# Optimization experiments

Measured on AMD Instinct MI355X. Metric: run time of the kernel, lower is better.

Reference implementation:

```python
import jax, jax.numpy as jnp
from jax import lax
import numpy as np

WS = 8        # window size
SHIFT = 4     # shift size
HEADS = 4
EPS = 1e-5


def _rel_pos_index(ws):
    coords = np.stack(np.meshgrid(np.arange(ws), np.arange(ws), indexing='ij'))  # (2,ws,ws)
    cf = coords.reshape(2, -1)
    rel = cf[:, :, None] - cf[:, None, :]           # (2,n,n)
    rel = rel.transpose(1, 2, 0).astype(np.int64)   # (n,n,2)
    rel[:, :, 0] += ws - 1
    rel[:, :, 1] += ws - 1
    rel[:, :, 0] *= 2 * ws - 1
    return rel.sum(-1)                              # (n,n)


def _attn_mask(h, w, ws, ss):
    img = np.zeros((h, w), dtype=np.float32)
    cnt = 0
    for hs in (slice(0, -ws), slice(-ws, -ss), slice(-ss, None)):
        for wsl in (slice(0, -ws), slice(-ws, -ss), slice(-ss, None)):
            img[hs, wsl] = cnt
            cnt += 1
    mw = img.reshape(h // ws, ws, w // ws, ws).transpose(0, 2, 1, 3).reshape(-1, ws * ws)
    am = mw[:, None, :] - mw[:, :, None]            # (nW,n,n)
    return np.where(am != 0, -100.0, 0.0).astype(np.float32)


def _ln(x, w, b):
    mu = x.mean(-1, keepdims=True)
    var = jnp.var(x, axis=-1, keepdims=True)
    return (x - mu) * lax.rsqrt(var + EPS) * w + b


def setup_inputs() -> dict:
    key = jax.random.key(0)
    ks = jax.random.split(key, 16)
    b, c, h, w = 4, 64, 256, 256
    hidden = 4 * c
    n_bias = (2 * WS - 1) * (2 * WS - 1)
    s = 0.02
    return {
        'x': jax.random.normal(ks[0], (b, c, h, w), jnp.float32),
        'norm1_w': jnp.ones((c,), jnp.float32),
        'norm1_b': jnp.zeros((c,), jnp.float32),
        'qkv_w': jax.random.normal(ks[1], (3 * c, c), jnp.float32) * s,
        'qkv_b': jnp.zeros((3 * c,), jnp.float32),
        'rpb': jax.random.normal(ks[2], (n_bias, HEADS), jnp.float32) * s,
        'proj_w': jax.random.normal(ks[3], (c, c), jnp.float32) * s,
        'proj_b': jnp.zeros((c,), jnp.float32),
        'norm2_w': jnp.ones((c,), jnp.float32),
        'norm2_b': jnp.zeros((c,), jnp.float32),
        'fc1_w': jax.random.normal(ks[4], (hidden, c), jnp.float32) * s,
        'fc1_b': jnp.zeros((hidden,), jnp.float32),
        'dw_w': jax.random.normal(ks[5], (hidden, 1, 5, 5), jnp.float32) * s,
        'dw_b': jnp.zeros((hidden,), jnp.float32),
        'fc2_w': jax.random.normal(ks[6], (c, hidden), jnp.float32) * s,
        'fc2_b': jnp.zeros((c,), jnp.float32),
    }


def reference(x, norm1_w, norm1_b, qkv_w, qkv_b, rpb, proj_w, proj_b,
              norm2_w, norm2_b, fc1_w, fc1_b, dw_w, dw_b, fc2_w, fc2_b):
    b, c, h, w = x.shape
    d = c // HEADS
    scale = d ** (-0.5)
    n = WS * WS

    x3 = jnp.transpose(x.reshape(b, c, h * w), (0, 2, 1))  # (b, hw, c)
    shortcut = x3
    xn = _ln(x3, norm1_w, norm1_b).reshape(b, h, w, c)

    # cyclic shift + window partition
    sx = jnp.roll(xn, (-SHIFT, -SHIFT), axis=(1, 2))
    win = sx.reshape(b, h // WS, WS, w // WS, WS, c).transpose(0, 1, 3, 2, 4, 5).reshape(-1, n, c)
    B_ = win.shape[0]

    qkv = (win @ qkv_w.T + qkv_b).reshape(B_, n, 3, HEADS, d).transpose(2, 0, 3, 1, 4)
    q, k, v = qkv[0] * scale, qkv[1], qkv[2]   # (B_, H, n, d)
    attn = jnp.einsum('bhnd,bhmd->bhnm', q, k)  # (B_, H, n, n)

    bias = rpb[jnp.asarray(_rel_pos_index(WS)).reshape(-1)].reshape(n, n, HEADS).transpose(2, 0, 1)
    attn = attn + bias[None]

    mask = jnp.asarray(_attn_mask(h, w, WS, SHIFT))  # (nW, n, n)
    nW = mask.shape[0]
    attn = attn.reshape(B_ // nW, nW, HEADS, n, n) + mask[None, :, None]
    attn = jax.nn.softmax(attn.reshape(B_, HEADS, n, n), axis=-1)

    out = jnp.einsum('bhnm,bhmd->bhnd', attn, v).transpose(0, 2, 1, 3).reshape(B_, n, c)
    out = out @ proj_w.T + proj_b

    # window reverse + un-shift
    sx = out.reshape(b, h // WS, w // WS, WS, WS, c).transpose(0, 1, 3, 2, 4, 5).reshape(b, h, w, c)
    xr = jnp.roll(sx, (SHIFT, SHIFT), axis=(1, 2)).reshape(b, h * w, c)
    x3 = shortcut + xr

    # ConvFFN
    xn = _ln(x3, norm2_w, norm2_b)
    hid = jax.nn.gelu(xn @ fc1_w.T + fc1_b, approximate=False)  # (b, hw, hidden)
    hidden = hid.shape[-1]
    himg = hid.transpose(0, 2, 1).reshape(b, hidden, h, w)
    dc = lax.conv_general_dilated(himg, dw_w, (1, 1), [(2, 2), (2, 2)],
                                  dimension_numbers=('NCHW', 'OIHW', 'NCHW'),
                                  feature_group_count=hidden)
    dc = jax.nn.gelu(dc + dw_b[None, :, None, None], approximate=False)
    hid = hid + dc.reshape(b, hidden, h * w).transpose(0, 2, 1)
    x3 = x3 + (hid @ fc2_w.T + fc2_b)

    return jnp.transpose(x3, (0, 2, 1)).reshape(b, c, h, w)
```

## Files before the change

### kernel.cpp

```cpp
#include <hip/hip_runtime.h>
#include <hip/hip_bf16.h>
#include <hip/hip_fp8.h>
#include <math.h>


typedef __bf16  bf16x8  __attribute__((ext_vector_type(8)));
typedef float   f32x4   __attribute__((ext_vector_type(4)));
typedef float   f32x2   __attribute__((ext_vector_type(2)));
typedef unsigned short ushortx8 __attribute__((ext_vector_type(8)));

__device__ __forceinline__ float gelu_f(float v) {
    float u = v * fmaf(0.0713548354f, v * v, 1.5957691216f);
    float t = __expf(u);
    float r = __builtin_amdgcn_rcpf(t + 1.0f);
    return v - v * r;
}
__device__ __forceinline__ unsigned char f32_to_fp8(float v) {
    __hip_fp8_e4m3 t(v);
    return (unsigned char)t.__x;
}
__device__ __forceinline__ float fp8_to_f32(unsigned char u) {
    __hip_fp8_e4m3 t;
    t.__x = (__hip_fp8_storage_t)u;
    return (float)t;
}

#if __has_builtin(__builtin_amdgcn_cvt_pk_f32_fp8) && __has_builtin(__builtin_amdgcn_cvt_pk_fp8_f32)
#define HW_FP8 1
#endif
template<bool HI>
__device__ __forceinline__ f32x2 fp8x2_f32(unsigned int u) {
#ifdef HW_FP8
    return __builtin_amdgcn_cvt_pk_f32_fp8((int)u, HI);
#else
    f32x2 r;
    const int s = HI ? 16 : 0;
    r.x = fp8_to_f32((unsigned char)(u >> s));
    r.y = fp8_to_f32((unsigned char)(u >> (s + 8)));
    return r;
#endif
}
template<bool HI>
__device__ __forceinline__ unsigned int f32x2_fp8(float a, float b, unsigned int old) {
#ifdef HW_FP8
    return (unsigned int)__builtin_amdgcn_cvt_pk_fp8_f32(a, b, (int)old, HI);
#else
    unsigned int v = (unsigned int)f32_to_fp8(a) | ((unsigned int)f32_to_fp8(b) << 8);
    return HI ? ((old & 0x0000ffffu) | (v << 16)) : ((old & 0xffff0000u) | v);
#endif
}

__device__ __forceinline__ unsigned short f2bf(float f) {
    unsigned int u = __builtin_bit_cast(unsigned int, f);
    u += 0x7fffu + ((u >> 16) & 1u);
    return (unsigned short)(u >> 16);
}
__device__ __forceinline__ float bf2f(unsigned short u) {
    return __builtin_bit_cast(float, ((unsigned int)u) << 16);
}
__device__ __forceinline__ unsigned int cvt_pk_bf16(float a, float b) {
#if defined(__gfx950__)
    unsigned int r;
    asm("v_cvt_pk_bf16_f32 %0, %1, %2" : "=v"(r) : "v"(a), "v"(b));
    return r;
#else
    return (unsigned int)f2bf(a) | ((unsigned int)f2bf(b) << 16);
#endif
}

__global__ __launch_bounds__(256) void k_prep(
        const float* __restrict__ qkvw, const float* __restrict__ projw,
        const float* __restrict__ rpb,  const float* __restrict__ fc1w,
        unsigned short* __restrict__ qkvw_bf, unsigned short* __restrict__ projw_bf,
        unsigned short* __restrict__ rpb_bf,  unsigned short* __restrict__ fc1w_bf) {
    const int i = blockIdx.x * 256 + threadIdx.x;
    if (i < 12288) qkvw_bf[i] = f2bf(qkvw[i]);
    if (i < 4096)  projw_bf[i] = f2bf(projw[i]);
    if (i < 900)   rpb_bf[i]   = f2bf(rpb[i]);
    if (i < 16384) fc1w_bf[i]  = f2bf(fc1w[i]);
}

__global__ __launch_bounds__(256) void k_cvt(const float* __restrict__ src,
        unsigned short* __restrict__ dst, int n) {
    const int i = blockIdx.x * 256 + threadIdx.x;
    if (i < n) dst[i] = f2bf(src[i]);
}

__global__ __launch_bounds__(256) void k_ln1(const float* __restrict__ x,
        const float* __restrict__ w1, const float* __restrict__ b1,
        unsigned short* __restrict__ A, unsigned short* __restrict__ Bw) {
    __shared__ float tile[64 * 65];
    __shared__ float red0[256], red1[256];
    __shared__ float muv[64], rsv[64], lw[64], lb[64];
    const int tid = threadIdx.x;
    const int gid = blockIdx.x;
    const int xc = gid & 3, y = (gid >> 2) & 255, b = gid >> 10;
    const int x0 = xc * 64;
    if (tid < 64) { lw[tid] = w1[tid]; lb[tid] = b1[tid]; }

    const float* xb = x + ((size_t)b * 64) * 65536 + y * 256 + x0;
    {
        const int tk = tid & 63, cl = tid >> 6;
        for (int it = 0; it < 16; ++it) {
            int cc = cl + 4 * it;
            tile[cc * 65 + tk] = xb[(size_t)cc * 65536 + tk];
        }
    }
    __syncthreads();
    {
        const int tk = tid & 63, cl = tid >> 6;
        float s = 0.f, s2 = 0.f;
        #pragma unroll
        for (int k = 0; k < 16; ++k) {
            float v = tile[(cl * 16 + k) * 65 + tk];
            s += v; s2 += v * v;
        }
        red0[cl * 64 + tk] = s; red1[cl * 64 + tk] = s2;
    }
    __syncthreads();
    if (tid < 64) {
        float s  = red0[tid] + red0[64 + tid] + red0[128 + tid] + red0[192 + tid];
        float s2 = red1[tid] + red1[64 + tid] + red1[128 + tid] + red1[192 + tid];
        float mu = s * (1.f / 64.f);
        float var = s2 * (1.f / 64.f) - mu * mu;
        muv[tid] = mu; rsv[tid] = rsqrtf(var + 1e-5f);
    }
    __syncthreads();
    const int cp = tid & 31, ch0 = cp * 2;
    const int tl = tid >> 5;
    const float2 lwp = *(const float2*)&lw[ch0];
    const float2 lbp = *(const float2*)&lb[ch0];
    const int ys = (y + 252) & 255;
    const int wy = ys >> 3, py = ys & 7;
    #pragma unroll
    for (int it = 0; it < 8; ++it) {
        const int t = tl + 8 * it;
        const float v0 = tile[ch0 * 65 + t];
        const float v1 = tile[(ch0 + 1) * 65 + t];
        const int tok = (b << 16) + y * 256 + x0 + t;
        *(unsigned int*)&A[(size_t)tok * 64 + ch0] = cvt_pk_bf16(v0, v1);
        const float mu = muv[t], rs = rsv[t];
        const float vn0 = (v0 - mu) * rs * lwp.x + lbp.x;
        const float vn1 = (v1 - mu) * rs * lwp.y + lbp.y;
        const int xs = (x0 + t + 252) & 255;
        const int wx = xs >> 3, px = xs & 7;
        const int widx = (b << 10) + (wy << 5) + wx;
        const int pos = (py << 3) + px;
        *(unsigned int*)&Bw[((size_t)widx * 64 + pos) * 64 + ch0] = cvt_pk_bf16(vn0, vn1);
    }
}

__global__ __launch_bounds__(256) void k_attn(
        const unsigned short* __restrict__ Bw,
        const unsigned short* __restrict__ qkvw_bf,
        const unsigned short* __restrict__ projw_bf,
        const unsigned short* __restrict__ rpb_bf,
        const float* __restrict__ qkvb,
        const float* __restrict__ projb,
        const unsigned short* __restrict__ A, unsigned short* __restrict__ Cb) {
    __shared__ __align__(16) unsigned short Xs[4608];
    __shared__ __align__(16) unsigned short Ws[13824];
    __shared__ __align__(8)  unsigned short rpbl[900];
    __shared__ float qkvbl[192];
    __shared__ float projbl[64];

    const int tid = threadIdx.x;
    const int lane = tid & 63, wv = tid >> 6;
    const int l15 = lane & 15, quad = lane >> 4;
    const int widx = blockIdx.x;
    const int wib = widx & 1023;
    const int wy = wib >> 5, wx = wib & 31, bimg = widx >> 10;
    const bool edge = (wy == 31) | (wx == 31);

    const f32x4 zz = {0.f, 0.f, 0.f, 0.f};
    const ushortx8 zu = {0, 0, 0, 0, 0, 0, 0, 0};
    const bf16x8 z8 = __builtin_bit_cast(bf16x8, zu);
    const ushortx8 ou = {0x3F80, 0x3F80, 0x3F80, 0x3F80, 0x3F80, 0x3F80, 0x3F80, 0x3F80};
    const bf16x8 ones8 = __builtin_bit_cast(bf16x8, ou);

    const ushortx8 pw0 = *(const ushortx8*)(projw_bf + tid * 8);
    const ushortx8 pw1 = *(const ushortx8*)(projw_bf + (256 + tid) * 8);

    {
        const unsigned short* Xg = Bw + (size_t)widx * 4096 + wv * 1024;
        #pragma unroll
        for (int it = 0; it < 2; ++it) {
            int g = it * 64 + lane;
            int row = g >> 3, c8 = g & 7;
            *(ushortx8*)&Xs[(wv * 16 + row) * 72 + c8 * 8] =
                *(const ushortx8*)(Xg + g * 8);
        }
    }
    #pragma unroll
    for (int it = 0; it < 6; ++it) {
        int g = it * 256 + tid;
        int row = g >> 3, c8 = g & 7;
        *(ushortx8*)&Ws[row * 72 + c8 * 8] = *(const ushortx8*)(qkvw_bf + g * 8);
    }
    if (tid < 225) *(uint2*)&rpbl[tid * 4] = *(const uint2*)(rpb_bf + tid * 4);
    if (tid < 192) qkvbl[tid] = qkvb[tid];
    if (tid < 64)  projbl[tid] = projb[tid];
    __syncthreads();

    f32x4 qacc[12];
    #pragma unroll
    for (int i = 0; i < 12; ++i) qacc[i] = zz;
    {
        const bf16x8 av0 = *(const bf16x8*)&Xs[(16 * wv + l15) * 72 + quad * 8];
        const bf16x8 av1 = *(const bf16x8*)&Xs[(16 * wv + l15) * 72 + 32 + quad * 8];
        #pragma unroll
        for (int gl = 0; gl < 12; ++gl) {
            bf16x8 bv0 = *(const bf16x8*)&Ws[(gl * 16 + l15) * 72 + quad * 8];
            qacc[gl] = __builtin_amdgcn_mfma_f32_16x16x32_bf16(av0, bv0, qacc[gl], 0, 0, 0);
            bf16x8 bv1 = *(const bf16x8*)&Ws[(gl * 16 + l15) * 72 + 32 + quad * 8];
            qacc[gl] = __builtin_amdgcn_mfma_f32_16x16x32_bf16(av1, bv1, qacc[gl], 0, 0, 0);
        }
    }
    __syncthreads();

    #pragma unroll
    for (int g = 0; g < 12; ++g) {
        #pragma unroll
        for (int r = 0; r < 4; ++r) {
            int tok = 16 * wv + quad * 4 + r;
            int oc  = g * 16 + l15;
            float v = qacc[g][r] + qkvbl[oc];
            if (g < 4)       Ws[g * 1024 + tok * 16 + l15] = f2bf(v * 0.25f);
            else if (g < 8)  Ws[4096 + (g - 4) * 1024 + tok * 16 + l15] = f2bf(v);
            else             Ws[8192 + ((g - 8) * 16 + l15) * 72 + tok] = f2bf(v);
        }
    }
    __syncthreads();

    f32x4 sacc[4][4];
    #pragma unroll
    for (int h = 0; h < 4; ++h) {
        bf16x8 qa = z8;
        if (quad < 2) qa = *(const bf16x8*)&Ws[h * 1024 + (16 * wv + l15) * 16 + quad * 8];
        #pragma unroll
        for (int nt = 0; nt < 4; ++nt) {
            bf16x8 kf = z8;
            if (quad < 2) kf = *(const bf16x8*)&Ws[4096 + h * 1024 + (nt * 16 + l15) * 16 + quad * 8];
            sacc[h][nt] = __builtin_amdgcn_mfma_f32_16x16x32_bf16(qa, kf, zz, 0, 0, 0);
        }
    }
    __syncthreads();

    {
        const int r0 = tid >> 3;
        *(ushortx8*)&Ws[4096 + r0 * 64 + (((tid & 7) ^ (r0 & 7)) << 3)] = pw0;
        const int g1 = 256 + tid, r1 = g1 >> 3;
        *(ushortx8*)&Ws[4096 + r1 * 64 + (((g1 & 7) ^ (r1 & 7)) << 3)] = pw1;
    }

    const int jhi = l15 >> 3, jlo = l15 & 7;
    int offj4[4], regj[4];
    #pragma unroll
    for (int nt = 0; nt < 4; ++nt) {
        int j = nt * 16 + l15;
        int jy = j >> 3, jx = j & 7;
        offj4[nt] = (jy * 15 + jx) * 4;
        regj[nt] = 0;
        if (edge) {
            int ysj = wy * 8 + jy, xsj = wx * 8 + jx;
            regj[nt] = (ysj >= 252 ? 2 : (ysj >= 248 ? 1 : 0)) * 3
                     + (xsj >= 252 ? 2 : (xsj >= 248 ? 1 : 0));
        }
    }
    int rbA[4], regiA[4], pbaseA[4], i7A[4];
    #pragma unroll
    for (int r = 0; r < 4; ++r) {
        const int i = 16 * wv + quad * 4 + r;
        const int iy = i >> 3, ix = i & 7;
        rbA[r] = ((iy + 7) * 15 + (ix + 7)) * 4;
        i7A[r] = i & 7;
        pbaseA[r] = i * 64 + jlo;
        regiA[r] = 0;
        if (edge) {
            const int ysi = wy * 8 + iy, xsi = wx * 8 + ix;
            regiA[r] = (ysi >= 252 ? 2 : (ysi >= 248 ? 1 : 0)) * 3
                     + (xsi >= 252 ? 2 : (xsi >= 248 ? 1 : 0));
        }
    }

    #pragma unroll
    for (int r = 0; r < 4; ++r) {
        #pragma unroll
        for (int nt = 0; nt < 4; ++nt) {
            const uint2 bw = *(const uint2*)&rpbl[rbA[r] - offj4[nt]];
            float mk = 0.f;
            if (edge) mk = (regj[nt] == regiA[r]) ? 0.f : -100.f;
            sacc[0][nt][r] += __builtin_bit_cast(float, bw.x << 16) + mk;
            sacc[1][nt][r] += __builtin_bit_cast(float, bw.x & 0xffff0000u) + mk;
            sacc[2][nt][r] += __builtin_bit_cast(float, bw.y << 16) + mk;
            sacc[3][nt][r] += __builtin_bit_cast(float, bw.y & 0xffff0000u) + mk;
        }
    }
    int pA_[4][4];
    #pragma unroll
    for (int r = 0; r < 4; ++r)
        #pragma unroll
        for (int nt = 0; nt < 4; ++nt)
            pA_[r][nt] = pbaseA[r] + ((((nt << 1) | jhi) ^ i7A[r]) << 3);

    f32x4 o[4];
    #pragma unroll
    for (int h = 0; h < 4; ++h) {
        #pragma unroll
        for (int r = 0; r < 4; ++r) {
            const unsigned int pk01 = cvt_pk_bf16(__expf(sacc[h][0][r]),
                                                  __expf(sacc[h][1][r]));
            const unsigned int pk23 = cvt_pk_bf16(__expf(sacc[h][2][r]),
                                                  __expf(sacc[h][3][r]));
            Ws[pA_[r][0]] = (unsigned short)pk01;
            Ws[pA_[r][1]] = (unsigned short)(pk01 >> 16);
            Ws[pA_[r][2]] = (unsigned short)pk23;
            Ws[pA_[r][3]] = (unsigned short)(pk23 >> 16);
        }
        o[h] = zz;
        f32x4 os = zz;
        #pragma unroll
        for (int s = 0; s < 2; ++s) {
            bf16x8 pa = *(const bf16x8*)&Ws[(16 * wv + l15) * 64
                                            + (((s * 4 + quad) ^ (l15 & 7)) << 3)];
            bf16x8 vb = *(const bf16x8*)&Ws[8192 + (h * 16 + l15) * 72 + s * 32 + quad * 8];
            o[h] = __builtin_amdgcn_mfma_f32_16x16x32_bf16(pa, vb, o[h], 0, 0, 0);
            os   = __builtin_amdgcn_mfma_f32_16x16x32_bf16(pa, ones8, os, 0, 0, 0);
        }
        #pragma unroll
        for (int r = 0; r < 4; ++r) o[h][r] *= __builtin_amdgcn_rcpf(os[r]);
    }

    unsigned short resid[16];
    #pragma unroll
    for (int r = 0; r < 4; ++r) {
        int tok = 16 * wv + quad * 4 + r;
        int py = tok >> 3, px = tok & 7;
        int yo = (wy * 8 + py + 4) & 255, xo = (wx * 8 + px + 4) & 255;
        size_t gt = ((size_t)bimg << 16) + yo * 256 + xo;
        #pragma unroll
        for (int nt = 0; nt < 4; ++nt)
            resid[r * 4 + nt] = A[gt * 64 + nt * 16 + l15];
    }

    #pragma unroll
    for (int h = 0; h < 4; ++h)
        #pragma unroll
        for (int r = 0; r < 4; ++r)
            Xs[(16 * wv + quad * 4 + r) * 72 + h * 16 + l15] = f2bf(o[h][r]);
    __syncthreads();

    f32x4 pacc[4];
    #pragma unroll
    for (int nt = 0; nt < 4; ++nt) {
        pacc[nt] = zz;
        #pragma unroll
        for (int s = 0; s < 2; ++s) {
            bf16x8 oa = *(const bf16x8*)&Xs[(16 * wv + l15) * 72 + s * 32 + quad * 8];
            bf16x8 wb = *(const bf16x8*)&Ws[4096 + (nt * 16 + l15) * 64
                                            + (((s * 4 + quad) ^ (l15 & 7)) << 3)];
            pacc[nt] = __builtin_amdgcn_mfma_f32_16x16x32_bf16(oa, wb, pacc[nt], 0, 0, 0);
        }
    }

    #pragma unroll
    for (int r = 0; r < 4; ++r) {
        int tok = 16 * wv + quad * 4 + r;
        int py = tok >> 3, px = tok & 7;
        int yo = (wy * 8 + py + 4) & 255, xo = (wx * 8 + px + 4) & 255;
        size_t gt = ((size_t)bimg << 16) + yo * 256 + xo;
        #pragma unroll
        for (int nt = 0; nt < 4; ++nt) {
            int oc = nt * 16 + l15;
            float v = pacc[nt][r] + projbl[oc] + bf2f(resid[r * 4 + nt]);
            Cb[gt * 64 + oc] = f2bf(v);
        }
    }
}

__global__ __launch_bounds__(256) void k_ln2fc1(const unsigned short* __restrict__ Cb,
        const float* __restrict__ w2, const float* __restrict__ b2,
        const unsigned short* __restrict__ fc1w_bf, const float* __restrict__ fc1b,
        unsigned char* __restrict__ D) {
    __shared__ __align__(16) unsigned short Xb[64 * 72];
    __shared__ __align__(16) unsigned short Wb[256 * 72];
    __shared__ float red0[256], red1[256];
    __shared__ float muv[64], rsv[64], lwv[64], lbv[64], fb[256];
    const int tid = threadIdx.x, gid = blockIdx.x;
    const int xc = gid & 3, y = (gid >> 2) & 255, b = gid >> 10;
    const int x0 = xc * 64;
    const int lane = tid & 63, wv = tid >> 6;
    const int l15 = lane & 15, quad = lane >> 4;
    const f32x4 zz = {0.f, 0.f, 0.f, 0.f};

    if (tid < 64) { lwv[tid] = w2[tid]; lbv[tid] = b2[tid]; }
    fb[tid] = fc1b[tid];

    const unsigned short* Cp = Cb + ((size_t)(b << 16) + y * 256 + x0) * 64;
    #pragma unroll
    for (int it = 0; it < 2; ++it) {
        const int g = it * 256 + tid;
        const int row = g >> 3, c8 = g & 7;
        *(ushortx8*)&Xb[row * 72 + c8 * 8] = *(const ushortx8*)(Cp + g * 8);
    }
    {
        const ushortx8* w8 = (const ushortx8*)fc1w_bf;
        #pragma unroll
        for (int it = 0; it < 8; ++it) {
            int idx = it * 256 + tid;
            int row = idx >> 3, c8 = idx & 7;
            *(ushortx8*)&Wb[row * 72 + c8 * 8] = w8[idx];
        }
    }
    __syncthreads();
    {
        const int tok = tid & 63, cl = tid >> 6;
        float s = 0.f, s2 = 0.f;
        #pragma unroll
        for (int g = 0; g < 2; ++g) {
            const ushortx8 u = *(const ushortx8*)&Xb[tok * 72 + cl * 16 + g * 8];
            #pragma unroll
            for (int k = 0; k < 8; ++k) { float v = bf2f(u[k]); s += v; s2 += v * v; }
        }
        red0[cl * 64 + tok] = s; red1[cl * 64 + tok] = s2;
    }
    __syncthreads();
    if (tid < 64) {
        float s  = red0[tid] + red0[64 + tid] + red0[128 + tid] + red0[192 + tid];
        float s2 = red1[tid] + red1[64 + tid] + red1[128 + tid] + red1[192 + tid];
        float mu = s * (1.f / 64.f);
        float var = s2 * (1.f / 64.f) - mu * mu;
        muv[tid] = mu; rsv[tid] = rsqrtf(var + 1e-5f);
    }
    __syncthreads();
    {
        const int c8n = tid & 7;
        const float4 lwa = *(const float4*)&lwv[c8n * 8];
        const float4 lwb2 = *(const float4*)&lwv[c8n * 8 + 4];
        const float4 lba = *(const float4*)&lbv[c8n * 8];
        const float4 lbb2 = *(const float4*)&lbv[c8n * 8 + 4];
        const float lw8[8] = {lwa.x, lwa.y, lwa.z, lwa.w, lwb2.x, lwb2.y, lwb2.z, lwb2.w};
        const float lb8[8] = {lba.x, lba.y, lba.z, lba.w, lbb2.x, lbb2.y, lbb2.z, lbb2.w};
        #pragma unroll
        for (int it = 0; it < 2; ++it) {
            const int row = it * 32 + (tid >> 3);
            const ushortx8 u = *(const ushortx8*)&Xb[row * 72 + c8n * 8];
            const float mu = muv[row], rs = rsv[row];
            float v[8];
            #pragma unroll
            for (int k = 0; k < 8; ++k) v[k] = (bf2f(u[k]) - mu) * rs * lw8[k] + lb8[k];
            uint4 pk;
            pk.x = cvt_pk_bf16(v[0], v[1]); pk.y = cvt_pk_bf16(v[2], v[3]);
            pk.z = cvt_pk_bf16(v[4], v[5]); pk.w = cvt_pk_bf16(v[6], v[7]);
            *(uint4*)&Xb[row * 72 + c8n * 8] = pk;
        }
    }
    __syncthreads();

    f32x4 acc[4][4];
    #pragma unroll
    for (int mt = 0; mt < 4; ++mt)
        #pragma unroll
        for (int nt = 0; nt < 4; ++nt) acc[mt][nt] = zz;
    #pragma unroll
    for (int s = 0; s < 2; ++s) {
        bf16x8 Bf[4];
        #pragma unroll
        for (int nt = 0; nt < 4; ++nt)
            Bf[nt] = *(const bf16x8*)&Xb[(nt * 16 + l15) * 72 + s * 32 + quad * 8];
        #pragma unroll
        for (int mt = 0; mt < 4; ++mt) {
            bf16x8 Af = *(const bf16x8*)&Wb[(64 * wv + 16 * mt + l15) * 72 + s * 32 + quad * 8];
            #pragma unroll
            for (int nt = 0; nt < 4; ++nt)
                acc[mt][nt] = __builtin_amdgcn_mfma_f32_16x16x32_bf16(Af, Bf[nt], acc[mt][nt], 0, 0, 0);
        }
    }

    unsigned int* stT = (unsigned int*)&Wb[(size_t)(64 * wv) * 72];
    const int s4 = lane >> 4;
    #pragma unroll
    for (int mt = 0; mt < 4; ++mt) {
        #pragma unroll
        for (int r = 0; r < 4; ++r) {
            const int mch = 64 * wv + 16 * mt + quad * 4 + r;
            const float bias = fb[mch];
            float g0 = gelu_f(acc[mt][0][r] + bias);
            float g1 = gelu_f(acc[mt][1][r] + bias);
            float g2 = gelu_f(acc[mt][2][r] + bias);
            float g3 = gelu_f(acc[mt][3][r] + bias);
            unsigned int pk = f32x2_fp8<false>(g0, g1, 0u);
            pk = f32x2_fp8<true>(g2, g3, pk);
            stT[(quad * 4 + r) * 20 + l15] = pk;
        }
        const int orow = l15;
        const uint4 w = *(const uint4*)&stT[orow * 20 + 4 * s4];
        const int mch2 = 64 * wv + 16 * mt + orow;
        unsigned char* Dp2 = D + (((size_t)(b * 256 + mch2)) << 16) + y * 256 + x0;
        #pragma unroll
        for (int p = 0; p < 4; ++p) {
            unsigned int o = ((w.x >> (8 * p)) & 0xffu)
                           | (((w.y >> (8 * p)) & 0xffu) << 8)
                           | (((w.z >> (8 * p)) & 0xffu) << 16)
                           | (((w.w >> (8 * p)) & 0xffu) << 24);
            *(unsigned int*)&Dp2[16 * p + 4 * s4] = o;
        }
    }
}

__global__ __launch_bounds__(256) void k_dwconv(const unsigned char* __restrict__ D,
        const float* __restrict__ dww, const float* __restrict__ dwb,
        unsigned char* __restrict__ E) {
    __shared__ __align__(16) unsigned short inT[36 * 280 + 16];
    __shared__ __align__(16) unsigned short Atab[5 * 64 * 8];
    __shared__ __align__(16) unsigned char outT[4][16 * 144];
    const int tid = threadIdx.x, gid = blockIdx.x;
    const int yt = gid & 7, pc = gid >> 3;
    const int ch = pc & 255;
    const int y0 = yt * 32;
    const unsigned char* Dp = D + ((size_t)pc << 16);
    const f32x4 zz = {0.f, 0.f, 0.f, 0.f};

    for (int idx = tid; idx < 432; idx += 256) {
        const int r = idx / 12, c = idx - r * 12;
        const int dw = (c == 0) ? 0 : (128 + c);
        ((unsigned int*)&inT[r * 280])[dw] = 0u;
    }
    #pragma unroll
    for (int it = 0; it < 9; ++it) {
        const int u = it * 256 + tid;
        const int t = u >> 6, c = u & 63;
        const int gy = y0 - 2 + t;
        unsigned int v = 0u;
        if ((unsigned)gy < 256u) v = *(const unsigned int*)(Dp + gy * 256 + 4 * c);
        const f32x2 lo = fp8x2_f32<false>(v);
        const f32x2 hi = fp8x2_f32<true>(v);
        unsigned int* base = (unsigned int*)&inT[t * 280 + 2 + 4 * c];
        base[0] = cvt_pk_bf16(lo.x, lo.y);
        base[1] = cvt_pk_bf16(hi.x, hi.y);
    }
    #pragma unroll
    for (int q = 0; q < 10; ++q) {
        const int e = tid * 10 + q;
        const int ky = e >> 9, r = e & 511;
        const int l = r >> 3, j = r & 7;
        const int m = l & 15, k = ((l >> 4) << 3) + j;
        const int d = k - m;
        float wv = 0.f;
        if (d >= 0 && d < 5) wv = dww[ch * 25 + ky * 5 + d];
        Atab[e] = f2bf(wv);
    }
    const float bb = dwb[ch];
    __syncthreads();

    const int wv_ = tid >> 6, lane = tid & 63;
    const int l15 = lane & 15, quad = lane >> 4;
    const int g = wv_ >> 1, xh = wv_ & 1;
    bf16x8 Af[5];
    #pragma unroll
    for (int ky = 0; ky < 5; ++ky)
        Af[ky] = *(const bf16x8*)&Atab[(ky * 64 + lane) * 8];
    const int tbase = g * 16 + l15;

    #pragma unroll
    for (int xp = 0; xp < 8; ++xp) {
        const int xs = xh * 128 + xp * 16;
        f32x4 acc = zz;
        #pragma unroll
        for (int ky = 0; ky < 5; ++ky) {
            bf16x8 Bf = *(const bf16x8*)&inT[(tbase + ky) * 280 + xs + quad * 8];
            acc = __builtin_amdgcn_mfma_f32_16x16x32_bf16(Af[ky], Bf, acc, 0, 0, 0);
        }
        const unsigned int* cp32 = (const unsigned int*)&inT[(tbase + 2) * 280 + 2 + xs + quad * 4];
        const unsigned int c01 = cp32[0], c23 = cp32[1];
        const float c0 = bf2f((unsigned short)c01), c1 = bf2f((unsigned short)(c01 >> 16));
        const float c2 = bf2f((unsigned short)c23), c3 = bf2f((unsigned short)(c23 >> 16));
        unsigned int pk = f32x2_fp8<false>(c0 + gelu_f(acc[0] + bb), c1 + gelu_f(acc[1] + bb), 0u);
        pk = f32x2_fp8<true>(c2 + gelu_f(acc[2] + bb), c3 + gelu_f(acc[3] + bb), pk);
        *(unsigned int*)&outT[wv_][l15 * 144 + xp * 16 + quad * 4] = pk;
    }

    {
        const int row = lane >> 2, sg = lane & 3;
        unsigned char* Ep = E + ((size_t)pc << 16) + (y0 + g * 16 + row) * 256 + xh * 128 + sg * 32;
        *(uint4*)Ep        = *(const uint4*)&outT[wv_][row * 144 + sg * 32];
        *(uint4*)(Ep + 16) = *(const uint4*)&outT[wv_][row * 144 + sg * 32 + 16];
    }
}

__global__ __launch_bounds__(256) void k_fc2(const unsigned char* __restrict__ E,
        const unsigned short* __restrict__ Cb, const unsigned short* __restrict__ fc2w_bf,
        const float* __restrict__ fc2b, float* __restrict__ out) {
    __shared__ __align__(16) unsigned short Hb[64 * 136];
    __shared__ __align__(16) unsigned short Wb2[64 * 264];
    __shared__ __align__(16) unsigned short Cl[64 * 72];
    __shared__ float fbl[64];
    const int tid = threadIdx.x, gid = blockIdx.x;
    const int xc = gid & 3, y = (gid >> 2) & 255, b = gid >> 10;
    const int x0 = xc * 64;
    const int lane = tid & 63, wv = tid >> 6;
    const int l15 = lane & 15, quad = lane >> 4;
    const f32x4 zz = {0.f, 0.f, 0.f, 0.f};

    if (tid < 64) fbl[tid] = fc2b[tid];
    {
        const unsigned short* Cp = Cb + ((size_t)(b << 16) + y * 256 + x0) * 64;
        #pragma unroll
        for (int it = 0; it < 2; ++it) {
            const int g = it * 256 + tid;
            const int row = g >> 3, c8 = g & 7;
            *(ushortx8*)&Cl[row * 72 + c8 * 8] = *(const ushortx8*)(Cp + g * 8);
        }
    }
    {
        const ushortx8* w8 = (const ushortx8*)fc2w_bf;
        #pragma unroll
        for (int it = 0; it < 8; ++it) {
            int idx = it * 256 + tid;
            int row = idx >> 5, c8 = idx & 31;
            *(ushortx8*)&Wb2[row * 264 + c8 * 8] = w8[idx];
        }
    }

    f32x4 acc[4];
    #pragma unroll
    for (int nt = 0; nt < 4; ++nt) acc[nt] = zz;

    const int ldc = tid >> 4;
    const int tq  = tid & 15;
    unsigned int u0[8];
    #pragma unroll
    for (int it = 0; it < 8; ++it) {
        int chl = ldc + 16 * it;
        u0[it] = *(const unsigned int*)&E[(((size_t)(b * 256 + chl)) << 16) + y * 256 + x0 + 4 * tq];
    }
    __syncthreads();

    for (int kc = 0; kc < 2; ++kc) {
        #pragma unroll
        for (int it = 0; it < 8; ++it) {
            int chl = ldc + 16 * it;
            f32x2 lo = fp8x2_f32<false>(u0[it]);
            f32x2 hi = fp8x2_f32<true>(u0[it]);
            const unsigned int p01 = cvt_pk_bf16(lo.x, lo.y);
            const unsigned int p23 = cvt_pk_bf16(hi.x, hi.y);
            unsigned short hs[4] = {(unsigned short)p01, (unsigned short)(p01 >> 16),
                                    (unsigned short)p23, (unsigned short)(p23 >> 16)};
            #pragma unroll
            for (int j = 0; j < 4; ++j) {
                int tok = 4 * tq + j;
                int p = (((chl >> 3) ^ (tok >> 2)) << 3) + (chl & 7);
                Hb[tok * 136 + p] = hs[j];
            }
        }
        if (kc == 0) {
            #pragma unroll
            for (int it = 0; it < 8; ++it) {
                int chl = ldc + 16 * it + 128;
                u0[it] = *(const unsigned int*)&E[(((size_t)(b * 256 + chl)) << 16) + y * 256 + x0 + 4 * tq];
            }
        }
        __syncthreads();
        #pragma unroll
        for (int k32 = 0; k32 < 4; ++k32) {
            bf16x8 Af = *(const bf16x8*)&Wb2[(16 * wv + l15) * 264 + kc * 128 + k32 * 32 + quad * 8];
            const int g = k32 * 4 + quad;
            #pragma unroll
            for (int nt = 0; nt < 4; ++nt) {
                const int tok = nt * 16 + l15;
                bf16x8 Bf = *(const bf16x8*)&Hb[tok * 136 + ((g ^ (tok >> 2)) << 3)];
                acc[nt] = __builtin_amdgcn_mfma_f32_16x16x32_bf16(Af, Bf, acc[nt], 0, 0, 0);
            }
        }
        if (kc == 0) __syncthreads();
    }

    #pragma unroll
    for (int r = 0; r < 4; ++r) {
        const int oc = 16 * wv + quad * 4 + r;
        const float bias = fbl[oc];
        float* op = out + (((size_t)(b * 64 + oc)) << 16) + y * 256 + x0;
        #pragma unroll
        for (int nt = 0; nt < 4; ++nt) {
            const int tok = nt * 16 + l15;
            op[tok] = acc[nt][r] + bias + bf2f(Cl[tok * 72 + oc]);
        }
    }
}

extern "C" void kernel_launch(void* const* d_in, const int* in_sizes, int n_in,
                              void* d_out, int out_size, void* d_ws, size_t ws_size,
                              hipStream_t stream) {
    const float* x     = (const float*)d_in[0];
    const float* n1w   = (const float*)d_in[1];
    const float* n1b   = (const float*)d_in[2];
    const float* qkvw  = (const float*)d_in[3];
    const float* qkvb  = (const float*)d_in[4];
    const float* rpb   = (const float*)d_in[5];
    const float* projw = (const float*)d_in[6];
    const float* projb = (const float*)d_in[7];
    const float* n2w   = (const float*)d_in[8];
    const float* n2b   = (const float*)d_in[9];
    const float* fc1w  = (const float*)d_in[10];
    const float* fc1b  = (const float*)d_in[11];
    const float* dww   = (const float*)d_in[12];
    const float* dwb   = (const float*)d_in[13];
    const float* fc2w  = (const float*)d_in[14];
    const float* fc2b  = (const float*)d_in[15];
    float* out = (float*)d_out;

    char* ws = (char*)d_ws;
    const size_t MB = 1048576;
    unsigned short* Cbuf = (unsigned short*)ws;
    unsigned short* Ab   = (unsigned short*)(ws + 32 * MB);
    unsigned short* Bwp  = (unsigned short*)(ws + 64 * MB);
    unsigned char*  Dh   = (unsigned char*)(ws + 32 * MB);
    unsigned char*  Eh   = (unsigned char*)(ws + 96 * MB);

    unsigned short* qkvw_bf = (unsigned short*)(ws + 96 * MB);
    unsigned short* projw_bf = (unsigned short*)(ws + 96 * MB + 24576);
    unsigned short* rpb_bf   = (unsigned short*)(ws + 96 * MB + 32768);
    unsigned short* fc1w_bf  = (unsigned short*)(ws + 96 * MB + 34816);
    unsigned short* fc2w_bf  = (unsigned short*)(ws + 32 * MB);

    k_prep  <<<64,    256, 0, stream>>>(qkvw, projw, rpb, fc1w,
                                        qkvw_bf, projw_bf, rpb_bf, fc1w_bf);
    k_ln1   <<<4096,  256, 0, stream>>>(x, n1w, n1b, Ab, Bwp);
    k_attn  <<<4096,  256, 0, stream>>>(Bwp, qkvw_bf, projw_bf, rpb_bf,
                                        qkvb, projb, Ab, Cbuf);
    k_ln2fc1<<<4096,  256, 0, stream>>>(Cbuf, n2w, n2b, fc1w_bf, fc1b, Dh);
    k_dwconv<<<8192,  256, 0, stream>>>(Dh, dww, dwb, Eh);
    k_cvt   <<<64,    256, 0, stream>>>(fc2w, fc2w_bf, 16384);
    k_fc2   <<<4096,  256, 0, stream>>>(Eh, Cbuf, fc2w_bf, fc2b, out);
}
```

Measured before the change: 360.1 us.

## Fuse LayerNorm1 and shifted-window gather into the attention kernel

Removes the separate k_ln1 pass. Each attention block now reads its shifted 8x8 window directly from the fp32 NCHW input, computes LayerNorm in shared memory, and keeps the raw fp32 values in registers as the residual. This drops the bf16 A and Bw intermediate buffers and their global write and read traffic, plus one launch. In exchange the attention kernel gains an extra LN phase with more barriers, and its input reads are now strided 16-byte fp32 loads across channel planes. The residual is also kept in fp32 rather than bf16, which changes numerics slightly.

New measurement: 380.3 us. 1.06x slower.

```diff
diff --git a/kernel.cpp b/kernel.cpp
--- a/kernel.cpp
+++ b/kernel.cpp
@@ -86,78 +86,15 @@
     if (i < n) dst[i] = f2bf(src[i]);
 }
 
-__global__ __launch_bounds__(256) void k_ln1(const float* __restrict__ x,
-        const float* __restrict__ w1, const float* __restrict__ b1,
-        unsigned short* __restrict__ A, unsigned short* __restrict__ Bw) {
-    __shared__ float tile[64 * 65];
-    __shared__ float red0[256], red1[256];
-    __shared__ float muv[64], rsv[64], lw[64], lb[64];
-    const int tid = threadIdx.x;
-    const int gid = blockIdx.x;
-    const int xc = gid & 3, y = (gid >> 2) & 255, b = gid >> 10;
-    const int x0 = xc * 64;
-    if (tid < 64) { lw[tid] = w1[tid]; lb[tid] = b1[tid]; }
-
-    const float* xb = x + ((size_t)b * 64) * 65536 + y * 256 + x0;
-    {
-        const int tk = tid & 63, cl = tid >> 6;
-        for (int it = 0; it < 16; ++it) {
-            int cc = cl + 4 * it;
-            tile[cc * 65 + tk] = xb[(size_t)cc * 65536 + tk];
-        }
-    }
-    __syncthreads();
-    {
-        const int tk = tid & 63, cl = tid >> 6;
-        float s = 0.f, s2 = 0.f;
-        #pragma unroll
-        for (int k = 0; k < 16; ++k) {
-            float v = tile[(cl * 16 + k) * 65 + tk];
-            s += v; s2 += v * v;
-        }
-        red0[cl * 64 + tk] = s; red1[cl * 64 + tk] = s2;
-    }
-    __syncthreads();
-    if (tid < 64) {
-        float s  = red0[tid] + red0[64 + tid] + red0[128 + tid] + red0[192 + tid];
-        float s2 = red1[tid] + red1[64 + tid] + red1[128 + tid] + red1[192 + tid];
-        float mu = s * (1.f / 64.f);
-        float var = s2 * (1.f / 64.f) - mu * mu;
-        muv[tid] = mu; rsv[tid] = rsqrtf(var + 1e-5f);
-    }
-    __syncthreads();
-    const int cp = tid & 31, ch0 = cp * 2;
-    const int tl = tid >> 5;
-    const float2 lwp = *(const float2*)&lw[ch0];
-    const float2 lbp = *(const float2*)&lb[ch0];
-    const int ys = (y + 252) & 255;
-    const int wy = ys >> 3, py = ys & 7;
-    #pragma unroll
-    for (int it = 0; it < 8; ++it) {
-        const int t = tl + 8 * it;
-        const float v0 = tile[ch0 * 65 + t];
-        const float v1 = tile[(ch0 + 1) * 65 + t];
-        const int tok = (b << 16) + y * 256 + x0 + t;
-        *(unsigned int*)&A[(size_t)tok * 64 + ch0] = cvt_pk_bf16(v0, v1);
-        const float mu = muv[t], rs = rsv[t];
-        const float vn0 = (v0 - mu) * rs * lwp.x + lbp.x;
-        const float vn1 = (v1 - mu) * rs * lwp.y + lbp.y;
-        const int xs = (x0 + t + 252) & 255;
-        const int wx = xs >> 3, px = xs & 7;
-        const int widx = (b << 10) + (wy << 5) + wx;
-        const int pos = (py << 3) + px;
-        *(unsigned int*)&Bw[((size_t)widx * 64 + pos) * 64 + ch0] = cvt_pk_bf16(vn0, vn1);
-    }
-}
-
 __global__ __launch_bounds__(256) void k_attn(
-        const unsigned short* __restrict__ Bw,
+        const float* __restrict__ x,
+        const float* __restrict__ n1w, const float* __restrict__ n1b,
         const unsigned short* __restrict__ qkvw_bf,
         const unsigned short* __restrict__ projw_bf,
         const unsigned short* __restrict__ rpb_bf,
         const float* __restrict__ qkvb,
         const float* __restrict__ projb,
-        const unsigned short* __restrict__ A, unsigned short* __restrict__ Cb) {
+        unsigned short* __restrict__ Cb) {
     __shared__ __align__(16) unsigned short Xs[4608];
     __shared__ __align__(16) unsigned short Ws[13824];
     __shared__ __align__(8)  unsigned short rpbl[900];
@@ -178,28 +115,92 @@
     const ushortx8 ou = {0x3F80, 0x3F80, 0x3F80, 0x3F80, 0x3F80, 0x3F80, 0x3F80, 0x3F80};
     const bf16x8 ones8 = __builtin_bit_cast(bf16x8, ou);
 
+    float* rawT = (float*)Ws;
+    float* red0 = (float*)Xs;
+    float* red1 = red0 + 256;
+    float* lnw  = qkvbl;
+    float* lnb  = qkvbl + 64;
+    float* rsv  = qkvbl + 128;
+    float* muv  = projbl;
+
+    float qb = 0.f, pb = 0.f;
+    if (tid < 192) qb = qkvb[tid];
+    if (tid < 64)  pb = projb[tid];
+    if (tid < 64)  { lnw[tid] = n1w[tid]; lnb[tid] = n1b[tid]; }
+
     const ushortx8 pw0 = *(const ushortx8*)(projw_bf + tid * 8);
     const ushortx8 pw1 = *(const ushortx8*)(projw_bf + (256 + tid) * 8);
 
-    {
-        const unsigned short* Xg = Bw + (size_t)widx * 4096 + wv * 1024;
-        #pragma unroll
-        for (int it = 0; it < 2; ++it) {
-            int g = it * 64 + lane;
-            int row = g >> 3, c8 = g & 7;
-            *(ushortx8*)&Xs[(wv * 16 + row) * 72 + c8 * 8] =
-                *(const ushortx8*)(Xg + g * 8);
-        }
-    }
+    if (tid < 225) *(uint2*)&rpbl[tid * 4] = *(const uint2*)(rpb_bf + tid * 4);
+
+    {
+        const float* xb = x + (((size_t)bimg * 64) << 16);
+        #pragma unroll
+        for (int it = 0; it < 4; ++it) {
+            const int u = it * 256 + tid;
+            const int ch = u >> 4, py = (u >> 1) & 7, half = u & 1;
+            const int iy = (wy * 8 + py + 4) & 255;
+            const int col0 = (wx * 8 + 4 + half * 4) & 255;
+            const float4 v = *(const float4*)(xb + ((size_t)ch << 16) + iy * 256 + col0);
+            f32x4 w4 = {v.x, v.y, v.z, v.w};
+            *(f32x4*)&rawT[ch * 68 + py * 8 + half * 4] = w4;
+        }
+    }
+    __syncthreads();
+
+    {
+        const int tk = tid & 63, cl = tid >> 6;
+        float s = 0.f, s2 = 0.f;
+        #pragma unroll
+        for (int k = 0; k < 16; ++k) {
+            float v = rawT[(cl * 16 + k) * 68 + tk];
+            s += v; s2 += v * v;
+        }
+        red0[cl * 64 + tk] = s; red1[cl * 64 + tk] = s2;
+    }
+    __syncthreads();
+    if (tid < 64) {
+        float s  = red0[tid] + red0[64 + tid] + red0[128 + tid] + red0[192 + tid];
+        float s2 = red1[tid] + red1[64 + tid] + red1[128 + tid] + red1[192 + tid];
+        float mu = s * (1.f / 64.f);
+        float var = s2 * (1.f / 64.f) - mu * mu;
+        muv[tid] = mu; rsv[tid] = rsqrtf(var + 1e-5f);
+    }
+    __syncthreads();
+
+    {
+        const int cp = tid & 31, ch0 = cp * 2, tl = tid >> 5;
+        const float lw0 = lnw[ch0], lw1 = lnw[ch0 + 1];
+        const float lb0 = lnb[ch0], lb1 = lnb[ch0 + 1];
+        #pragma unroll
+        for (int it = 0; it < 8; ++it) {
+            const int t = tl + 8 * it;
+            const float v0 = rawT[ch0 * 68 + t];
+            const float v1 = rawT[(ch0 + 1) * 68 + t];
+            const float mu = muv[t], rs = rsv[t];
+            const float vn0 = (v0 - mu) * rs * lw0 + lb0;
+            const float vn1 = (v1 - mu) * rs * lw1 + lb1;
+            *(unsigned int*)&Xs[t * 72 + ch0] = cvt_pk_bf16(vn0, vn1);
+        }
+    }
+    float residf[16];
+    #pragma unroll
+    for (int r = 0; r < 4; ++r) {
+        const int tok = 16 * wv + quad * 4 + r;
+        #pragma unroll
+        for (int nt = 0; nt < 4; ++nt)
+            residf[r * 4 + nt] = rawT[(nt * 16 + l15) * 68 + tok];
+    }
+    __syncthreads();
+
+    if (tid < 192) qkvbl[tid] = qb;
+    if (tid < 64)  projbl[tid] = pb;
     #pragma unroll
     for (int it = 0; it < 6; ++it) {
         int g = it * 256 + tid;
         int row = g >> 3, c8 = g & 7;
         *(ushortx8*)&Ws[row * 72 + c8 * 8] = *(const ushortx8*)(qkvw_bf + g * 8);
     }
-    if (tid < 225) *(uint2*)&rpbl[tid * 4] = *(const uint2*)(rpb_bf + tid * 4);
-    if (tid < 192) qkvbl[tid] = qkvb[tid];
-    if (tid < 64)  projbl[tid] = projb[tid];
     __syncthreads();
 
     f32x4 qacc[12];
@@ -331,7 +332,26 @@
         for (int r = 0; r < 4; ++r) o[h][r] *= __builtin_amdgcn_rcpf(os[r]);
     }
 
-    unsigned short resid[16];
+    #pragma unroll
+    for (int h = 0; h < 4; ++h)
+        #pragma unroll
+        for (int r = 0; r < 4; ++r)
+            Xs[(16 * wv + quad * 4 + r) * 72 + h * 16 + l15] = f2bf(o[h][r]);
+    __syncthreads();
+
+    f32x4 pacc[4];
+    #pragma unroll
+    for (int nt = 0; nt < 4; ++nt) {
+        pacc[nt] = zz;
+        #pragma unroll
+        for (int s = 0; s < 2; ++s) {
+            bf16x8 oa = *(const bf16x8*)&Xs[(16 * wv + l15) * 72 + s * 32 + quad * 8];
+            bf16x8 wb = *(const bf16x8*)&Ws[4096 + (nt * 16 + l15) * 64
+                                            + (((s * 4 + quad) ^ (l15 & 7)) << 3)];
+            pacc[nt] = __builtin_amdgcn_mfma_f32_16x16x32_bf16(oa, wb, pacc[nt], 0, 0, 0);
+        }
+    }
+
     #pragma unroll
     for (int r = 0; r < 4; ++r) {
         int tok = 16 * wv + quad * 4 + r;
@@ -339,40 +359,9 @@
         int yo = (wy * 8 + py + 4) & 255, xo = (wx * 8 + px + 4) & 255;
         size_t gt = ((size_t)bimg << 16) + yo * 256 + xo;
         #pragma unroll
-        for (int nt = 0; nt < 4; ++nt)
-            resid[r * 4 + nt] = A[gt * 64 + nt * 16 + l15];
-    }
-
-    #pragma unroll
-    for (int h = 0; h < 4; ++h)
-        #pragma unroll
-        for (int r = 0; r < 4; ++r)
-            Xs[(16 * wv + quad * 4 + r) * 72 + h * 16 + l15] = f2bf(o[h][r]);
-    __syncthreads();
-
-    f32x4 pacc[4];
-    #pragma unroll
-    for (int nt = 0; nt < 4; ++nt) {
-        pacc[nt] = zz;
-        #pragma unroll
-        for (int s = 0; s < 2; ++s) {
-            bf16x8 oa = *(const bf16x8*)&Xs[(16 * wv + l15) * 72 + s * 32 + quad * 8];
-            bf16x8 wb = *(const bf16x8*)&Ws[4096 + (nt * 16 + l15) * 64
-                                            + (((s * 4 + quad) ^ (l15 & 7)) << 3)];
-            pacc[nt] = __builtin_amdgcn_mfma_f32_16x16x32_bf16(oa, wb, pacc[nt], 0, 0, 0);
-        }
-    }
-
-    #pragma unroll
-    for (int r = 0; r < 4; ++r) {
-        int tok = 16 * wv + quad * 4 + r;
-        int py = tok >> 3, px = tok & 7;
-        int yo = (wy * 8 + py + 4) & 255, xo = (wx * 8 + px + 4) & 255;
-        size_t gt = ((size_t)bimg << 16) + yo * 256 + xo;
-        #pragma unroll
         for (int nt = 0; nt < 4; ++nt) {
             int oc = nt * 16 + l15;
-            float v = pacc[nt][r] + projbl[oc] + bf2f(resid[r * 4 + nt]);
+            float v = pacc[nt][r] + projbl[oc] + residf[r * 4 + nt];
             Cb[gt * 64 + oc] = f2bf(v);
         }
     }
@@ -712,8 +701,6 @@
     char* ws = (char*)d_ws;
     const size_t MB = 1048576;
     unsigned short* Cbuf = (unsigned short*)ws;
-    unsigned short* Ab   = (unsigned short*)(ws + 32 * MB);
-    unsigned short* Bwp  = (unsigned short*)(ws + 64 * MB);
     unsigned char*  Dh   = (unsigned char*)(ws + 32 * MB);
     unsigned char*  Eh   = (unsigned char*)(ws + 96 * MB);
 
@@ -725,9 +712,8 @@
 
     k_prep  <<<64,    256, 0, stream>>>(qkvw, projw, rpb, fc1w,
                                         qkvw_bf, projw_bf, rpb_bf, fc1w_bf);
-    k_ln1   <<<4096,  256, 0, stream>>>(x, n1w, n1b, Ab, Bwp);
-    k_attn  <<<4096,  256, 0, stream>>>(Bwp, qkvw_bf, projw_bf, rpb_bf,
-                                        qkvb, projb, Ab, Cbuf);
+    k_attn  <<<4096,  256, 0, stream>>>(x, n1w, n1b, qkvw_bf, projw_bf, rpb_bf,
+                                        qkvb, projb, Cbuf);
     k_ln2fc1<<<4096,  256, 0, stream>>>(Cbuf, n2w, n2b, fc1w_bf, fc1b, Dh);
     k_dwconv<<<8192,  256, 0, stream>>>(Dh, dww, dwb, Eh);
     k_cvt   <<<64,    256, 0, stream>>>(fc2w, fc2w_bf, 16384);
```
